# Performance work log

Measured on AMD Instinct MI355X. Metric: run time of the kernel, lower is better.

The kernel has to match this reference:

```python
import jax, jax.numpy as jnp
import numpy as np

IN_FEATURES = 4096
OUT_FEATURES = 11008
TOKENS = 32


def ternarize_weight(w):
    # abs-mean scale, clamped; threshold at 0.7*abs_mean
    abs_mean = jnp.maximum(jnp.mean(jnp.abs(w)), 1e-5)
    threshold = 0.7 * abs_mean
    q = jnp.where(w > threshold, 1.0, jnp.where(w < -threshold, -1.0, 0.0))
    # straight-through estimator: forward value q*abs_mean, grad passes to w
    return w + jax.lax.stop_gradient(q * abs_mean - w)


def setup_inputs() -> dict:
    key = jax.random.key(0)
    kx, kw = jax.random.split(key)
    x = jax.random.normal(kx, (TOKENS, IN_FEATURES), dtype=jnp.float32)
    # master fp32 weights, init std = 1/sqrt(in_features) as in the module
    weight = jax.random.normal(kw, (OUT_FEATURES, IN_FEATURES), dtype=jnp.float32) / np.sqrt(IN_FEATURES)
    return {"x": x, "weight": weight}


def reference(x, weight):
    # ternary_active=True, ternary_alpha=1.0 path: fully ternarized weights
    w_q = ternarize_weight(weight)
    # F.linear(x, w): [T, in] @ [out, in]^T -> [T, out]
    return jnp.einsum('ti,oi->to', x, w_q)
```

## Files before the change

kernel.cpp:

```cpp
#include <hip/hip_runtime.h>
#include <hip/hip_bf16.h>
#include <stdint.h>

#define IN_F 4096
#define OUT_F 11008
#define TOKENS 32
#define NELEM_W (OUT_F * IN_F)
#define OUT_ELEMS (TOKENS * OUT_F)

typedef __attribute__((ext_vector_type(8))) __bf16 bf16x8;
typedef __attribute__((ext_vector_type(4))) float  f32x4;

#define XB_OFF    64
#define GPART_OFF 262208
#define APART_OFF 3080256

__device__ __forceinline__ uint32_t bfr(float v) {
    uint32_t u = __float_as_uint(v);
    uint32_t r = u + 0x7FFFu + ((u >> 16) & 1u);
    return r >> 16;
}

#define ABSUM_BLOCKS 2048
#define XCVT_BLOCKS  64

__global__ __launch_bounds__(256) void absum_xcvt_kernel(const float* __restrict__ w,
                                                         const float* __restrict__ x,
                                                         float* __restrict__ apart,
                                                         uint4* __restrict__ xb) {
    if (blockIdx.x >= ABSUM_BLOCKS) {
        int i = (blockIdx.x - ABSUM_BLOCKS) * 256 + threadIdx.x;
        const float4* x4 = (const float4*)x;
        float4 a0 = x4[i * 2];
        float4 a1 = x4[i * 2 + 1];
        uint4 o;
        o.x = bfr(a0.x) | (bfr(a0.y) << 16);
        o.y = bfr(a0.z) | (bfr(a0.w) << 16);
        o.z = bfr(a1.x) | (bfr(a1.y) << 16);
        o.w = bfr(a1.z) | (bfr(a1.w) << 16);
        xb[i] = o;
        return;
    }
    int tid = blockIdx.x * blockDim.x + threadIdx.x;
    int stride = ABSUM_BLOCKS * 256;
    const float4* w4 = (const float4*)w;
    const int n4 = NELEM_W / 4;
    float s = 0.f;
    for (int i = tid; i < n4; i += stride) {
        float4 v = w4[i];
        s += fabsf(v.x) + fabsf(v.y) + fabsf(v.z) + fabsf(v.w);
    }
    for (int off = 32; off > 0; off >>= 1)
        s += __shfl_down(s, off, 64);
    __shared__ float wsum[4];
    int lane = threadIdx.x & 63;
    int wv   = threadIdx.x >> 6;
    if (lane == 0) wsum[wv] = s;
    __syncthreads();
    if (threadIdx.x == 0)
        apart[blockIdx.x] = wsum[0] + wsum[1] + wsum[2] + wsum[3];
}

__global__ __launch_bounds__(256) void finalize_kernel(const float* __restrict__ apart,
                                                       float* __restrict__ wsf) {
    float s = 0.f;
#pragma unroll
    for (int j = 0; j < 8; ++j)
        s += apart[threadIdx.x + 256 * j];
    for (int off = 32; off > 0; off >>= 1)
        s += __shfl_down(s, off, 64);
    __shared__ float wsum[4];
    int lane = threadIdx.x & 63;
    int wv   = threadIdx.x >> 6;
    if (lane == 0) wsum[wv] = s;
    __syncthreads();
    if (threadIdx.x == 0) {
        double mean = (double)(wsum[0] + wsum[1] + wsum[2] + wsum[3]) / (double)NELEM_W;
        if (mean < 1e-5) mean = 1e-5;
        float mf = (float)mean;
        wsf[2] = 0.7f * mf;
        wsf[3] = mf;
    }
}

__device__ __forceinline__ uint32_t tern1(float v, float thr) {
    uint32_t u  = __float_as_uint(v);
    uint32_t pm = (u & 0x80000000u) | 0x3F800000u;
    return (__builtin_fabsf(v) > thr) ? pm : 0u;
}

__device__ __forceinline__ uint2 tern4(float4 b, float thr) {
    uint32_t q0 = tern1(b.x, thr), q1 = tern1(b.y, thr);
    uint32_t q2 = tern1(b.z, thr), q3 = tern1(b.w, thr);
    uint2 r;
    r.x = __builtin_amdgcn_perm(q1, q0, 0x07060302u);
    r.y = __builtin_amdgcn_perm(q3, q2, 0x07060302u);
    return r;
}

#define CHUNKS 16
#define WAVE_LDS 2304
#define SMEM_BYTES 4608

__global__ __launch_bounds__(128, 4) void ternary_gemm(const float* __restrict__ w,
                                                       const float* __restrict__ wsf,
                                                       const __bf16* __restrict__ xb,
                                                       float* __restrict__ gpart) {
    __shared__ char smem_raw[SMEM_BYTES];
    const float thr = wsf[2];
    const int og   = blockIdx.x >> 1;
    const int kh   = blockIdx.x & 1;
    const int tid  = threadIdx.x;
    const int wv   = tid >> 6;
    const int lane = tid & 63;
    const int col  = lane & 15;
    const int quad = lane >> 4;
    const int rlan = lane & 15;

    const int kw = kh * 2048 + wv * 1024;

    const float* wp = w + (size_t)(og * 16 + quad) * IN_F + kw + rlan * 4;
    char* stage = smem_raw + wv * WAVE_LDS;
    char* wr    = stage + quad * 144 + rlan * 8;
    const char* rd = stage + col * 144;
    const __bf16* xq = xb + (size_t)col * IN_F + kw + quad * 8;

    f32x4 acc0 = {0.f, 0.f, 0.f, 0.f};
    f32x4 acc1 = {0.f, 0.f, 0.f, 0.f};

    float4 wb[2][4];
    bf16x8 xv[2][4];

#pragma unroll
    for (int c = 0; c < 2; ++c) {
        const float*  np = wp + c * 64;
        const __bf16* xn = xq + c * 64;
        wb[c][0] = *(const float4*)(np);
        wb[c][1] = *(const float4*)(np + 4 * IN_F);
        wb[c][2] = *(const float4*)(np + 8 * IN_F);
        wb[c][3] = *(const float4*)(np + 12 * IN_F);
        xv[c][0] = *(const bf16x8*)(xn);
        xv[c][1] = *(const bf16x8*)(xn + 32);
        xv[c][2] = *(const bf16x8*)(xn + 16 * IN_F);
        xv[c][3] = *(const bf16x8*)(xn + 16 * IN_F + 32);
    }

#define GEMM_BODY(c, cur)                                                      \
    {                                                                          \
        uint2 t0 = tern4(wb[cur][0], thr);                                     \
        uint2 t1 = tern4(wb[cur][1], thr);                                     \
        uint2 t2 = tern4(wb[cur][2], thr);                                     \
        uint2 t3 = tern4(wb[cur][3], thr);                                     \
        *(uint2*)(wr)        = t0;                                             \
        *(uint2*)(wr + 576)  = t1;                                             \
        *(uint2*)(wr + 1152) = t2;                                             \
        *(uint2*)(wr + 1728) = t3;                                             \
        bf16x8 a00 = xv[cur][0], a01 = xv[cur][1];                             \
        bf16x8 a10 = xv[cur][2], a11 = xv[cur][3];                             \
        if ((c) + 2 < CHUNKS) {                                                \
            const float*  np = wp + ((c) + 2) * 64;                            \
            const __bf16* xn = xq + ((c) + 2) * 64;                            \
            wb[cur][0] = *(const float4*)(np);                                 \
            wb[cur][1] = *(const float4*)(np + 4 * IN_F);                      \
            wb[cur][2] = *(const float4*)(np + 8 * IN_F);                      \
            wb[cur][3] = *(const float4*)(np + 12 * IN_F);                     \
            xv[cur][0] = *(const bf16x8*)(xn);                                 \
            xv[cur][1] = *(const bf16x8*)(xn + 32);                            \
            xv[cur][2] = *(const bf16x8*)(xn + 16 * IN_F);                     \
            xv[cur][3] = *(const bf16x8*)(xn + 16 * IN_F + 32);                \
        }                                                                      \
        bf16x8 bw0 = *(const bf16x8*)(rd + quad * 16);                         \
        bf16x8 bw1 = *(const bf16x8*)(rd + 64 + quad * 16);                    \
        acc0 = __builtin_amdgcn_mfma_f32_16x16x32_bf16(a00, bw0, acc0, 0, 0, 0); \
        acc1 = __builtin_amdgcn_mfma_f32_16x16x32_bf16(a10, bw0, acc1, 0, 0, 0); \
        acc0 = __builtin_amdgcn_mfma_f32_16x16x32_bf16(a01, bw1, acc0, 0, 0, 0); \
        acc1 = __builtin_amdgcn_mfma_f32_16x16x32_bf16(a11, bw1, acc1, 0, 0, 0); \
    }

    for (int c = 0; c < CHUNKS; c += 2) {
        GEMM_BODY(c, 0)
        GEMM_BODY(c + 1, 1)
    }
#undef GEMM_BODY

    __syncthreads();
    float* red  = (float*)smem_raw;
    float* base = red + wv * 512;
#pragma unroll
    for (int r = 0; r < 4; ++r) base[r * 64 + lane]       = acc0[r];
#pragma unroll
    for (int r = 0; r < 4; ++r) base[256 + r * 64 + lane] = acc1[r];
    __syncthreads();

    float* gp = gpart + (size_t)kh * OUT_ELEMS;
    for (int p = tid; p < 512; p += 128) {
        int t = p >> 4, cc = p & 15;
        int a = t >> 4;
        int q = (t >> 2) & 3;
        int r = t & 3;
        int idx = a * 256 + r * 64 + q * 16 + cc;
        gp[(size_t)t * OUT_F + og * 16 + cc] = red[idx] + red[512 + idx];
    }
}

__global__ __launch_bounds__(256) void combine_kernel(const float* __restrict__ gpart,
                                                      const float* __restrict__ wsf,
                                                      float* __restrict__ out) {
    const float sc = wsf[3];
    int i = blockIdx.x * 256 + threadIdx.x;
    const float4* p0 = (const float4*)gpart;
    const float4* p1 = (const float4*)(gpart + OUT_ELEMS);
    float4 a = p0[i], b = p1[i];
    float4 o;
    o.x = (a.x + b.x) * sc;
    o.y = (a.y + b.y) * sc;
    o.z = (a.z + b.z) * sc;
    o.w = (a.w + b.w) * sc;
    ((float4*)out)[i] = o;
}

extern "C" void kernel_launch(void* const* d_in, const int* in_sizes, int n_in,
                              void* d_out, int out_size, void* d_ws, size_t ws_size,
                              hipStream_t stream) {
    const float* x = (const float*)d_in[0];
    const float* w = (const float*)d_in[1];
    float* out     = (float*)d_out;
    char* ws       = (char*)d_ws;

    float* wsf     = (float*)ws;
    uint4* xb      = (uint4*)(ws + XB_OFF);
    float* gpart   = (float*)(ws + GPART_OFF);
    float* apart   = (float*)(ws + APART_OFF);

    absum_xcvt_kernel<<<ABSUM_BLOCKS + XCVT_BLOCKS, 256, 0, stream>>>(w, x, apart, xb);
    finalize_kernel<<<1, 256, 0, stream>>>(apart, wsf);
    ternary_gemm<<<(OUT_F / 16) * 2, 128, 0, stream>>>(w, wsf, (const __bf16*)(ws + XB_OFF), gpart);
    combine_kernel<<<OUT_ELEMS / 4 / 256, 256, 0, stream>>>(gpart, wsf, out);
}
```

Measured before the change: 280.8 us.

## Fuse abs-mean reduction into GEMM using sampled threshold and exception fixup

Drops the separate full pass over the fp32 weights that computed the abs-mean. The threshold is now estimated from a 1M-element sample, and the GEMM ternarizes with that estimate while also accumulating the exact abs sum. Weights within a narrow band around the estimated threshold are logged to an exception list. A fixup kernel then applies atomic corrections to outputs wherever the exact threshold flips the quantized value, and the k-split is removed so the block covers all of K. This trades the second weight read for per-element band checks, LDS atomics and a bounded exception buffer; results would be wrong if the true threshold falls outside the band or the buffer overflows.

```diff
diff --git a/kernel.cpp b/kernel.cpp
--- a/kernel.cpp
+++ b/kernel.cpp
@@ -13,7 +13,13 @@
 
 #define XB_OFF    64
 #define GPART_OFF 262208
-#define APART_OFF 3080256
+#define APART_OFF 1671232
+#define EXC_OFF   1675264
+#define EXC_CAP   262144u
+#define EXC_LOC   1024
+
+#define N_SAMPLE_F 1048576.0f
+#define DELTA 0.004f
 
 __device__ __forceinline__ uint32_t bfr(float v) {
     uint32_t u = __float_as_uint(v);
@@ -21,15 +27,18 @@
     return r >> 16;
 }
 
-#define ABSUM_BLOCKS 2048
-#define XCVT_BLOCKS  64
-
-__global__ __launch_bounds__(256) void absum_xcvt_kernel(const float* __restrict__ w,
-                                                         const float* __restrict__ x,
-                                                         float* __restrict__ apart,
-                                                         uint4* __restrict__ xb) {
-    if (blockIdx.x >= ABSUM_BLOCKS) {
-        int i = (blockIdx.x - ABSUM_BLOCKS) * 256 + threadIdx.x;
+__device__ __forceinline__ float thr_hat_from(float ssum) {
+    float m = ssum * (1.0f / N_SAMPLE_F);
+    if (m < 1e-5f) m = 1e-5f;
+    return 0.7f * m;
+}
+
+__global__ __launch_bounds__(256) void sample_xcvt_kernel(const float* __restrict__ w,
+                                                          const float* __restrict__ x,
+                                                          float* __restrict__ wsf,
+                                                          uint4* __restrict__ xb) {
+    if (blockIdx.x >= 256) {
+        int i = (blockIdx.x - 256) * 256 + threadIdx.x;
         const float4* x4 = (const float4*)x;
         float4 a0 = x4[i * 2];
         float4 a1 = x4[i * 2 + 1];
@@ -41,46 +50,23 @@
         xb[i] = o;
         return;
     }
-    int tid = blockIdx.x * blockDim.x + threadIdx.x;
-    int stride = ABSUM_BLOCKS * 256;
+    const int wv   = threadIdx.x >> 6;
+    const int lane = threadIdx.x & 63;
+    const int wid  = blockIdx.x * 4 + wv;
     const float4* w4 = (const float4*)w;
-    const int n4 = NELEM_W / 4;
+    size_t base = (size_t)wid * 11008 + lane;
     float s = 0.f;
-    for (int i = tid; i < n4; i += stride) {
-        float4 v = w4[i];
-        s += fabsf(v.x) + fabsf(v.y) + fabsf(v.z) + fabsf(v.w);
-    }
-    for (int off = 32; off > 0; off >>= 1)
-        s += __shfl_down(s, off, 64);
-    __shared__ float wsum[4];
-    int lane = threadIdx.x & 63;
-    int wv   = threadIdx.x >> 6;
-    if (lane == 0) wsum[wv] = s;
-    __syncthreads();
-    if (threadIdx.x == 0)
-        apart[blockIdx.x] = wsum[0] + wsum[1] + wsum[2] + wsum[3];
-}
-
-__global__ __launch_bounds__(256) void finalize_kernel(const float* __restrict__ apart,
-                                                       float* __restrict__ wsf) {
-    float s = 0.f;
-#pragma unroll
-    for (int j = 0; j < 8; ++j)
-        s += apart[threadIdx.x + 256 * j];
-    for (int off = 32; off > 0; off >>= 1)
-        s += __shfl_down(s, off, 64);
-    __shared__ float wsum[4];
-    int lane = threadIdx.x & 63;
-    int wv   = threadIdx.x >> 6;
-    if (lane == 0) wsum[wv] = s;
-    __syncthreads();
-    if (threadIdx.x == 0) {
-        double mean = (double)(wsum[0] + wsum[1] + wsum[2] + wsum[3]) / (double)NELEM_W;
-        if (mean < 1e-5) mean = 1e-5;
-        float mf = (float)mean;
-        wsf[2] = 0.7f * mf;
-        wsf[3] = mf;
-    }
+#pragma unroll
+    for (int r = 0; r < 4; ++r) {
+        float4 v = w4[base + (size_t)r * 2752];
+        s += __builtin_fabsf(v.x) + __builtin_fabsf(v.y) +
+             __builtin_fabsf(v.z) + __builtin_fabsf(v.w);
+    }
+    for (int off = 32; off > 0; off >>= 1) s += __shfl_down(s, off, 64);
+    __shared__ float ws4[4];
+    if (lane == 0) ws4[wv] = s;
+    __syncthreads();
+    if (threadIdx.x == 0) atomicAdd(&wsf[0], ws4[0] + ws4[1] + ws4[2] + ws4[3]);
 }
 
 __device__ __forceinline__ uint32_t tern1(float v, float thr) {
@@ -100,16 +86,26 @@
 
 #define CHUNKS 16
 #define WAVE_LDS 2304
-#define SMEM_BYTES 4608
-
-__global__ __launch_bounds__(128, 4) void ternary_gemm(const float* __restrict__ w,
+#define STAGE_BYTES 9216
+
+__global__ __launch_bounds__(256, 3) void ternary_gemm(const float* __restrict__ w,
                                                        const float* __restrict__ wsf,
                                                        const __bf16* __restrict__ xb,
-                                                       float* __restrict__ gpart) {
-    __shared__ char smem_raw[SMEM_BYTES];
-    const float thr = wsf[2];
-    const int og   = blockIdx.x >> 1;
-    const int kh   = blockIdx.x & 1;
+                                                       float* __restrict__ gpart,
+                                                       float* __restrict__ apart,
+                                                       uint2* __restrict__ excg,
+                                                       unsigned int* __restrict__ exc_cnt) {
+    __shared__ char smem_raw[STAGE_BYTES];
+    __shared__ uint2 exc_lds[EXC_LOC];
+    __shared__ unsigned int exc_n;
+    __shared__ unsigned int exc_base_s;
+    __shared__ float wsum4[4];
+
+    const float th = thr_hat_from(wsf[0]);
+    const float lo = th * (1.0f - DELTA);
+    const float hi = th * (1.0f + DELTA);
+
+    const int og   = blockIdx.x;
     const int tid  = threadIdx.x;
     const int wv   = tid >> 6;
     const int lane = tid & 63;
@@ -117,9 +113,13 @@
     const int quad = lane >> 4;
     const int rlan = lane & 15;
 
-    const int kw = kh * 2048 + wv * 1024;
-
-    const float* wp = w + (size_t)(og * 16 + quad) * IN_F + kw + rlan * 4;
+    if (tid == 0) exc_n = 0u;
+    __syncthreads();
+
+    const int kw    = wv * 1024;
+    const int obase = og * 16 + quad;
+
+    const float* wp = w + (size_t)obase * IN_F + kw + rlan * 4;
     char* stage = smem_raw + wv * WAVE_LDS;
     char* wr    = stage + quad * 144 + rlan * 8;
     const char* rd = stage + col * 144;
@@ -127,6 +127,7 @@
 
     f32x4 acc0 = {0.f, 0.f, 0.f, 0.f};
     f32x4 acc1 = {0.f, 0.f, 0.f, 0.f};
+    float sab = 0.f;
 
     float4 wb[2][4];
     bf16x8 xv[2][4];
@@ -145,12 +146,42 @@
         xv[c][3] = *(const bf16x8*)(xn + 16 * IN_F + 32);
     }
 
+#define WCHECK(f, oo, ii)                                                      \
+    {                                                                          \
+        float a_ = __builtin_fabsf(f);                                         \
+        if (a_ > lo && a_ < hi) {                                              \
+            unsigned int p_ = atomicAdd(&exc_n, 1u);                           \
+            if (p_ < (unsigned int)EXC_LOC) {                                  \
+                uint2 e_;                                                      \
+                e_.x = __float_as_uint(f);                                     \
+                e_.y = (unsigned int)((oo) * 4096 + (ii));                     \
+                exc_lds[p_] = e_;                                              \
+            }                                                                  \
+        }                                                                      \
+    }
+
+#define PROC4(vv, rr, cc)                                                      \
+    {                                                                          \
+        sab += __builtin_fabsf(vv.x) + __builtin_fabsf(vv.y) +                 \
+               __builtin_fabsf(vv.z) + __builtin_fabsf(vv.w);                  \
+        int o_  = obase + 4 * (rr);                                            \
+        int ib_ = kw + (cc) * 64 + rlan * 4;                                   \
+        WCHECK(vv.x, o_, ib_ + 0)                                              \
+        WCHECK(vv.y, o_, ib_ + 1)                                              \
+        WCHECK(vv.z, o_, ib_ + 2)                                              \
+        WCHECK(vv.w, o_, ib_ + 3)                                              \
+    }
+
 #define GEMM_BODY(c, cur)                                                      \
     {                                                                          \
-        uint2 t0 = tern4(wb[cur][0], thr);                                     \
-        uint2 t1 = tern4(wb[cur][1], thr);                                     \
-        uint2 t2 = tern4(wb[cur][2], thr);                                     \
-        uint2 t3 = tern4(wb[cur][3], thr);                                     \
+        uint2 t0 = tern4(wb[cur][0], th);                                      \
+        uint2 t1 = tern4(wb[cur][1], th);                                      \
+        uint2 t2 = tern4(wb[cur][2], th);                                      \
+        uint2 t3 = tern4(wb[cur][3], th);                                      \
+        PROC4(wb[cur][0], 0, c)                                                \
+        PROC4(wb[cur][1], 1, c)                                                \
+        PROC4(wb[cur][2], 2, c)                                                \
+        PROC4(wb[cur][3], 3, c)                                                \
         *(uint2*)(wr)        = t0;                                             \
         *(uint2*)(wr + 576)  = t1;                                             \
         *(uint2*)(wr + 1152) = t2;                                             \
@@ -182,40 +213,105 @@
         GEMM_BODY(c + 1, 1)
     }
 #undef GEMM_BODY
-
-    __syncthreads();
-    float* red  = (float*)smem_raw;
-    float* base = red + wv * 512;
-#pragma unroll
-    for (int r = 0; r < 4; ++r) base[r * 64 + lane]       = acc0[r];
-#pragma unroll
-    for (int r = 0; r < 4; ++r) base[256 + r * 64 + lane] = acc1[r];
-    __syncthreads();
-
-    float* gp = gpart + (size_t)kh * OUT_ELEMS;
-    for (int p = tid; p < 512; p += 128) {
-        int t = p >> 4, cc = p & 15;
+#undef PROC4
+#undef WCHECK
+
+    __syncthreads();
+    unsigned int nloc = exc_n;
+    if (nloc > (unsigned int)EXC_LOC) nloc = (unsigned int)EXC_LOC;
+
+    for (int off = 32; off > 0; off >>= 1) sab += __shfl_down(sab, off, 64);
+    if (lane == 0) wsum4[wv] = sab;
+    if (tid == 0) exc_base_s = atomicAdd(exc_cnt, nloc);
+    __syncthreads();
+    if (tid == 0) apart[og] = wsum4[0] + wsum4[1] + wsum4[2] + wsum4[3];
+
+    unsigned int gb = exc_base_s;
+    for (unsigned int e = tid; e < nloc; e += 256) {
+        unsigned int g = gb + e;
+        if (g < EXC_CAP) excg[g] = exc_lds[e];
+    }
+
+    float* red   = (float*)smem_raw;
+    float* basef = red + wv * 512;
+#pragma unroll
+    for (int r = 0; r < 4; ++r) basef[r * 64 + lane]       = acc0[r];
+#pragma unroll
+    for (int r = 0; r < 4; ++r) basef[256 + r * 64 + lane] = acc1[r];
+    __syncthreads();
+
+    for (int p = tid; p < 512; p += 256) {
+        int t = p >> 4, cc2 = p & 15;
         int a = t >> 4;
         int q = (t >> 2) & 3;
         int r = t & 3;
-        int idx = a * 256 + r * 64 + q * 16 + cc;
-        gp[(size_t)t * OUT_F + og * 16 + cc] = red[idx] + red[512 + idx];
-    }
-}
-
-__global__ __launch_bounds__(256) void combine_kernel(const float* __restrict__ gpart,
-                                                      const float* __restrict__ wsf,
-                                                      float* __restrict__ out) {
+        int idx = a * 256 + r * 64 + q * 16 + cc2;
+        gpart[(size_t)t * OUT_F + og * 16 + cc2] =
+            red[idx] + red[512 + idx] + red[1024 + idx] + red[1536 + idx];
+    }
+}
+
+__global__ __launch_bounds__(256) void finalize_kernel(const float* __restrict__ apart,
+                                                       float* __restrict__ wsf) {
+    float s = 0.f;
+#pragma unroll
+    for (int j = 0; j < 3; ++j) {
+        int k = threadIdx.x + 256 * j;
+        if (k < 688) s += apart[k];
+    }
+    for (int off = 32; off > 0; off >>= 1) s += __shfl_down(s, off, 64);
+    __shared__ float wsum[4];
+    int lane = threadIdx.x & 63;
+    int wv   = threadIdx.x >> 6;
+    if (lane == 0) wsum[wv] = s;
+    __syncthreads();
+    if (threadIdx.x == 0) {
+        double mean = (double)(wsum[0] + wsum[1] + wsum[2] + wsum[3]) / (double)NELEM_W;
+        if (mean < 1e-5) mean = 1e-5;
+        float mf = (float)mean;
+        wsf[2] = 0.7f * mf;
+        wsf[3] = mf;
+    }
+}
+
+__global__ __launch_bounds__(256) void fixup_kernel(const uint2* __restrict__ excg,
+                                                    const float* __restrict__ wsf,
+                                                    const unsigned int* __restrict__ exc_cnt,
+                                                    const __bf16* __restrict__ xb,
+                                                    float* __restrict__ gpart) {
+    const float thr = wsf[2];
+    const float th  = thr_hat_from(wsf[0]);
+    unsigned int n = *exc_cnt;
+    if (n > EXC_CAP) n = EXC_CAP;
+    for (unsigned int g = blockIdx.x * 256 + threadIdx.x; g < n; g += gridDim.x * 256) {
+        uint2 e = excg[g];
+        float v = __uint_as_float(e.x);
+        float a = __builtin_fabsf(v);
+        bool qt = a > thr;
+        bool qh = a > th;
+        if (qt != qh) {
+            float sgn = (e.x & 0x80000000u) ? -1.0f : 1.0f;
+            float d   = qt ? sgn : -sgn;
+            unsigned int o = e.y >> 12;
+            unsigned int i = e.y & 4095u;
+            const __bf16* xp = xb + i;
+            for (int t = 0; t < TOKENS; ++t)
+                atomicAdd(&gpart[(size_t)t * OUT_F + o], d * (float)xp[(size_t)t * IN_F]);
+        }
+    }
+}
+
+__global__ __launch_bounds__(256) void scale_kernel(const float* __restrict__ gpart,
+                                                    const float* __restrict__ wsf,
+                                                    float* __restrict__ out) {
     const float sc = wsf[3];
     int i = blockIdx.x * 256 + threadIdx.x;
-    const float4* p0 = (const float4*)gpart;
-    const float4* p1 = (const float4*)(gpart + OUT_ELEMS);
-    float4 a = p0[i], b = p1[i];
+    float4 a = ((const float4*)gpart)[i];
     float4 o;
-    o.x = (a.x + b.x) * sc;
-    o.y = (a.y + b.y) * sc;
-    o.z = (a.z + b.z) * sc;
-    o.w = (a.w + b.w) * sc;
+    o.x = a.x * sc;
+    o.y = a.y * sc;
+    o.z = a.z * sc;
+    o.w = a.w * sc;
     ((float4*)out)[i] = o;
 }
 
@@ -227,13 +323,19 @@
     float* out     = (float*)d_out;
     char* ws       = (char*)d_ws;
 
-    float* wsf     = (float*)ws;
-    uint4* xb      = (uint4*)(ws + XB_OFF);
-    float* gpart   = (float*)(ws + GPART_OFF);
-    float* apart   = (float*)(ws + APART_OFF);
-
-    absum_xcvt_kernel<<<ABSUM_BLOCKS + XCVT_BLOCKS, 256, 0, stream>>>(w, x, apart, xb);
+    float*        wsf   = (float*)ws;
+    unsigned int* wsu   = (unsigned int*)ws;
+    uint4*        xb    = (uint4*)(ws + XB_OFF);
+    float*        gpart = (float*)(ws + GPART_OFF);
+    float*        apart = (float*)(ws + APART_OFF);
+    uint2*        excg  = (uint2*)(ws + EXC_OFF);
+
+    hipMemsetAsync(ws, 0, 64, stream);
+    sample_xcvt_kernel<<<320, 256, 0, stream>>>(w, x, wsf, xb);
+    ternary_gemm<<<OUT_F / 16, 256, 0, stream>>>(w, wsf, (const __bf16*)(ws + XB_OFF),
+                                                 gpart, apart, excg, wsu + 1);
     finalize_kernel<<<1, 256, 0, stream>>>(apart, wsf);
-    ternary_gemm<<<(OUT_F / 16) * 2, 128, 0, stream>>>(w, wsf, (const __bf16*)(ws + XB_OFF), gpart);
-    combine_kernel<<<OUT_ELEMS / 4 / 256, 256, 0, stream>>>(gpart, wsf, out);
-}
+    fixup_kernel<<<256, 256, 0, stream>>>(excg, wsf, wsu + 1,
+                                          (const __bf16*)(ws + XB_OFF), gpart);
+    scale_kernel<<<OUT_ELEMS / 4 / 256, 256, 0, stream>>>(gpart, wsf, out);
+}
```

Result: slower. 315.4 us (+12.3%).

## Speculate ternary threshold from weight sample, then correct near-threshold weights

Applied to the files above, without the earlier changes.

Estimates the abs-mean threshold from a strided sample of about 1M weights, so the ternary GEMM can run before the full reduction finishes. A later pass computes the exact abs-sum and records weight groups whose magnitude lies within a small band of the estimated threshold. A fixup kernel then uses atomics to apply a rank-1 correction for every element whose ternary value differs under the exact threshold. The full weight read is still done twice, and the change adds a memset, an extra kernel and atomic traffic. Correctness relies on the exact threshold falling inside the detection band.

```diff
diff --git a/kernel.cpp b/kernel.cpp
--- a/kernel.cpp
+++ b/kernel.cpp
@@ -12,8 +12,14 @@
 typedef __attribute__((ext_vector_type(4))) float  f32x4;
 
 #define XB_OFF    64
-#define GPART_OFF 262208
-#define APART_OFF 3080256
+#define APART_OFF 262208
+#define GPART_OFF 270400
+#define EXC_OFF   3088448
+#define EXC_CAP   1048576u
+
+#define N_SAMPLE_F 1048576.0f
+#define DELTA 0.004f
+#define DET_BLOCKS 2048
 
 __device__ __forceinline__ uint32_t bfr(float v) {
     uint32_t u = __float_as_uint(v);
@@ -21,15 +27,18 @@
     return r >> 16;
 }
 
-#define ABSUM_BLOCKS 2048
-#define XCVT_BLOCKS  64
-
-__global__ __launch_bounds__(256) void absum_xcvt_kernel(const float* __restrict__ w,
-                                                         const float* __restrict__ x,
-                                                         float* __restrict__ apart,
-                                                         uint4* __restrict__ xb) {
-    if (blockIdx.x >= ABSUM_BLOCKS) {
-        int i = (blockIdx.x - ABSUM_BLOCKS) * 256 + threadIdx.x;
+__device__ __forceinline__ float thr_hat_from(float ssum) {
+    float m = ssum * (1.0f / N_SAMPLE_F);
+    if (m < 1e-5f) m = 1e-5f;
+    return 0.7f * m;
+}
+
+__global__ __launch_bounds__(256) void sample_xcvt_kernel(const float* __restrict__ w,
+                                                          const float* __restrict__ x,
+                                                          float* __restrict__ wsf,
+                                                          uint4* __restrict__ xb) {
+    if (blockIdx.x >= 256) {
+        int i = (blockIdx.x - 256) * 256 + threadIdx.x;
         const float4* x4 = (const float4*)x;
         float4 a0 = x4[i * 2];
         float4 a1 = x4[i * 2 + 1];
@@ -41,46 +50,23 @@
         xb[i] = o;
         return;
     }
-    int tid = blockIdx.x * blockDim.x + threadIdx.x;
-    int stride = ABSUM_BLOCKS * 256;
+    const int wv   = threadIdx.x >> 6;
+    const int lane = threadIdx.x & 63;
+    const int wid  = blockIdx.x * 4 + wv;
     const float4* w4 = (const float4*)w;
-    const int n4 = NELEM_W / 4;
+    size_t base = (size_t)wid * 11008 + lane;
     float s = 0.f;
-    for (int i = tid; i < n4; i += stride) {
-        float4 v = w4[i];
-        s += fabsf(v.x) + fabsf(v.y) + fabsf(v.z) + fabsf(v.w);
-    }
-    for (int off = 32; off > 0; off >>= 1)
-        s += __shfl_down(s, off, 64);
-    __shared__ float wsum[4];
-    int lane = threadIdx.x & 63;
-    int wv   = threadIdx.x >> 6;
-    if (lane == 0) wsum[wv] = s;
-    __syncthreads();
-    if (threadIdx.x == 0)
-        apart[blockIdx.x] = wsum[0] + wsum[1] + wsum[2] + wsum[3];
-}
-
-__global__ __launch_bounds__(256) void finalize_kernel(const float* __restrict__ apart,
-                                                       float* __restrict__ wsf) {
-    float s = 0.f;
-#pragma unroll
-    for (int j = 0; j < 8; ++j)
-        s += apart[threadIdx.x + 256 * j];
-    for (int off = 32; off > 0; off >>= 1)
-        s += __shfl_down(s, off, 64);
-    __shared__ float wsum[4];
-    int lane = threadIdx.x & 63;
-    int wv   = threadIdx.x >> 6;
-    if (lane == 0) wsum[wv] = s;
-    __syncthreads();
-    if (threadIdx.x == 0) {
-        double mean = (double)(wsum[0] + wsum[1] + wsum[2] + wsum[3]) / (double)NELEM_W;
-        if (mean < 1e-5) mean = 1e-5;
-        float mf = (float)mean;
-        wsf[2] = 0.7f * mf;
-        wsf[3] = mf;
-    }
+#pragma unroll
+    for (int r = 0; r < 4; ++r) {
+        float4 v = w4[base + (size_t)r * 2752];
+        s += __builtin_fabsf(v.x) + __builtin_fabsf(v.y) +
+             __builtin_fabsf(v.z) + __builtin_fabsf(v.w);
+    }
+    for (int off = 32; off > 0; off >>= 1) s += __shfl_down(s, off, 64);
+    __shared__ float ws4[4];
+    if (lane == 0) ws4[wv] = s;
+    __syncthreads();
+    if (threadIdx.x == 0) atomicAdd(&wsf[0], ws4[0] + ws4[1] + ws4[2] + ws4[3]);
 }
 
 __device__ __forceinline__ uint32_t tern1(float v, float thr) {
@@ -107,7 +93,7 @@
                                                        const __bf16* __restrict__ xb,
                                                        float* __restrict__ gpart) {
     __shared__ char smem_raw[SMEM_BYTES];
-    const float thr = wsf[2];
+    const float thr = thr_hat_from(wsf[0]);
     const int og   = blockIdx.x >> 1;
     const int kh   = blockIdx.x & 1;
     const int tid  = threadIdx.x;
@@ -203,10 +189,116 @@
     }
 }
 
+__global__ __launch_bounds__(256) void absum_detect(const float* __restrict__ w,
+                                                    const float* __restrict__ wsf,
+                                                    float* __restrict__ apart,
+                                                    unsigned int* __restrict__ excg,
+                                                    unsigned int* __restrict__ exc_cnt) {
+    __shared__ unsigned int ebuf[512];
+    __shared__ unsigned int en;
+    __shared__ unsigned int ebase;
+    __shared__ float wsum[4];
+    if (threadIdx.x == 0) en = 0u;
+    __syncthreads();
+
+    const float th  = thr_hat_from(wsf[0]);
+    const float eps = th * DELTA;
+
+    int tid = blockIdx.x * blockDim.x + threadIdx.x;
+    int stride = DET_BLOCKS * 256;
+    const float4* w4 = (const float4*)w;
+    const int n4 = NELEM_W / 4;
+    float s = 0.f;
+    for (int i = tid; i < n4; i += stride) {
+        float4 v = w4[i];
+        float ax = __builtin_fabsf(v.x), ay = __builtin_fabsf(v.y);
+        float az = __builtin_fabsf(v.z), aw = __builtin_fabsf(v.w);
+        s += ax + ay + az + aw;
+        int h = (__builtin_fabsf(ax - th) < eps) | (__builtin_fabsf(ay - th) < eps) |
+                (__builtin_fabsf(az - th) < eps) | (__builtin_fabsf(aw - th) < eps);
+        if (h) {
+            unsigned int p = atomicAdd(&en, 1u);
+            if (p < 512u) ebuf[p] = (unsigned int)i;
+        }
+    }
+    for (int off = 32; off > 0; off >>= 1) s += __shfl_down(s, off, 64);
+    int lane = threadIdx.x & 63;
+    int wv   = threadIdx.x >> 6;
+    if (lane == 0) wsum[wv] = s;
+    __syncthreads();
+    if (threadIdx.x == 0) {
+        apart[blockIdx.x] = wsum[0] + wsum[1] + wsum[2] + wsum[3];
+        unsigned int n = en > 512u ? 512u : en;
+        ebase = atomicAdd(exc_cnt, n);
+    }
+    __syncthreads();
+    unsigned int n = en > 512u ? 512u : en;
+    unsigned int gb = ebase;
+    for (unsigned int e = threadIdx.x; e < n; e += 256) {
+        unsigned int g = gb + e;
+        if (g < EXC_CAP) excg[g] = ebuf[e];
+    }
+}
+
+__global__ __launch_bounds__(256) void finalize_kernel(const float* __restrict__ apart,
+                                                       float* __restrict__ wsf) {
+    float s = 0.f;
+#pragma unroll
+    for (int j = 0; j < 8; ++j)
+        s += apart[threadIdx.x + 256 * j];
+    for (int off = 32; off > 0; off >>= 1) s += __shfl_down(s, off, 64);
+    __shared__ float wsum[4];
+    int lane = threadIdx.x & 63;
+    int wv   = threadIdx.x >> 6;
+    if (lane == 0) wsum[wv] = s;
+    __syncthreads();
+    if (threadIdx.x == 0) {
+        double mean = (double)(wsum[0] + wsum[1] + wsum[2] + wsum[3]) / (double)NELEM_W;
+        if (mean < 1e-5) mean = 1e-5;
+        float mf = (float)mean;
+        wsf[4] = 0.7f * mf;
+        wsf[5] = mf;
+    }
+}
+
+__global__ __launch_bounds__(128) void fixup_kernel(const unsigned int* __restrict__ excg,
+                                                    const float* __restrict__ w,
+                                                    const float* __restrict__ wsf,
+                                                    const unsigned int* __restrict__ exc_cnt,
+                                                    const __bf16* __restrict__ xb,
+                                                    float* __restrict__ gpart) {
+    const float th  = thr_hat_from(wsf[0]);
+    const float thr = wsf[4];
+    unsigned int n = *exc_cnt;
+    if (n > EXC_CAP) n = EXC_CAP;
+    const float4* w4 = (const float4*)w;
+    for (unsigned int g = blockIdx.x * 128 + threadIdx.x; g < n; g += gridDim.x * 128) {
+        unsigned int idx4 = excg[g];
+        float4 v4 = w4[idx4];
+        unsigned int o     = idx4 >> 10;
+        unsigned int ibase = (idx4 & 1023u) * 4u;
+        float el[4] = {v4.x, v4.y, v4.z, v4.w};
+#pragma unroll
+        for (int e = 0; e < 4; ++e) {
+            float v = el[e];
+            float a = __builtin_fabsf(v);
+            bool qt = a > thr;
+            bool qh = a > th;
+            if (qt != qh) {
+                float sgn = (__float_as_uint(v) & 0x80000000u) ? -1.0f : 1.0f;
+                float d   = qt ? sgn : -sgn;
+                const __bf16* xp = xb + (ibase + e);
+                for (int t = 0; t < TOKENS; ++t)
+                    atomicAdd(&gpart[(size_t)t * OUT_F + o], d * (float)xp[(size_t)t * IN_F]);
+            }
+        }
+    }
+}
+
 __global__ __launch_bounds__(256) void combine_kernel(const float* __restrict__ gpart,
                                                       const float* __restrict__ wsf,
                                                       float* __restrict__ out) {
-    const float sc = wsf[3];
+    const float sc = wsf[5];
     int i = blockIdx.x * 256 + threadIdx.x;
     const float4* p0 = (const float4*)gpart;
     const float4* p1 = (const float4*)(gpart + OUT_ELEMS);
@@ -227,13 +319,19 @@
     float* out     = (float*)d_out;
     char* ws       = (char*)d_ws;
 
-    float* wsf     = (float*)ws;
-    uint4* xb      = (uint4*)(ws + XB_OFF);
-    float* gpart   = (float*)(ws + GPART_OFF);
-    float* apart   = (float*)(ws + APART_OFF);
-
-    absum_xcvt_kernel<<<ABSUM_BLOCKS + XCVT_BLOCKS, 256, 0, stream>>>(w, x, apart, xb);
+    float*        wsf   = (float*)ws;
+    unsigned int* wsu   = (unsigned int*)ws;
+    uint4*        xb    = (uint4*)(ws + XB_OFF);
+    float*        apart = (float*)(ws + APART_OFF);
+    float*        gpart = (float*)(ws + GPART_OFF);
+    unsigned int* excg  = (unsigned int*)(ws + EXC_OFF);
+
+    hipMemsetAsync(ws, 0, 64, stream);
+    sample_xcvt_kernel<<<320, 256, 0, stream>>>(w, x, wsf, xb);
+    ternary_gemm<<<1376, 128, 0, stream>>>(w, wsf, (const __bf16*)(ws + XB_OFF), gpart);
+    absum_detect<<<DET_BLOCKS, 256, 0, stream>>>(w, wsf, apart, excg, wsu + 1);
     finalize_kernel<<<1, 256, 0, stream>>>(apart, wsf);
-    ternary_gemm<<<(OUT_F / 16) * 2, 128, 0, stream>>>(w, wsf, (const __bf16*)(ws + XB_OFF), gpart);
-    combine_kernel<<<OUT_ELEMS / 4 / 256, 256, 0, stream>>>(gpart, wsf, out);
-}
+    fixup_kernel<<<512, 128, 0, stream>>>(excg, w, wsf, wsu + 1,
+                                          (const __bf16*)(ws + XB_OFF), gpart);
+    combine_kernel<<<344, 256, 0, stream>>>(gpart, wsf, out);
+}
```

Result: slower. 448.1 us (+59.6%).
